# Kernel tuning notes

Measured on AMD Instinct MI355X. Metric: run time of the kernel, lower is better.

## Reference

```python
import jax, jax.numpy as jnp
import numpy as np

K = 3  # kernel_size
P = K // 2


def setup_inputs() -> dict:
    key = jax.random.key(0)
    k1, k2 = jax.random.split(key)
    x = jax.random.normal(k1, (8, 64, 256, 256), dtype=jnp.float32)
    alpha = jnp.full((1, 64, 1, 1), 0.1, dtype=jnp.float32)
    return {"x": x, "alpha": alpha}


def reference(x, alpha):
    # Equivalent to F.unfold(x, K, padding=P) -> abs-diff from center -> sum over K*K -> residual.
    b, c, h, w = x.shape
    xp = jnp.pad(x, ((0, 0), (0, 0), (P, P), (P, P)))  # zero padding, same as F.unfold
    diff_sum = jnp.zeros_like(x)
    for di in range(K):
        for dj in range(K):
            neighbor = xp[:, :, di:di + h, dj:dj + w]
            diff_sum = diff_sum + jnp.abs(x - neighbor)
    return x + alpha * diff_sum
```

## Files before the change

### kernel.cpp

```cpp
#include <hip/hip_runtime.h>


constexpr int H = 256;
constexpr int W = 256;
constexpr int C = 64;

__global__ __launch_bounds__(256, 4) void adc_kernel(
    const float* __restrict__ x,
    const float* __restrict__ alpha,
    float* __restrict__ out)
{
    const int lane = threadIdx.x & 63;
    const int wave = threadIdx.x >> 6;
    const int slab = blockIdx.x;
    const int img  = slab >> 4;
    const int s16  = slab & 15;
    const int y0   = s16 * 16 + wave * 4;
    const int c    = img & (C - 1);

    const float  a    = alpha[c];
    const float* imgp = x   + (long)img * (H * W);
    float*       outp = out + (long)img * (H * W);
    const int    w0   = lane * 4;
    const float* base = imgp + (long)y0 * W + w0;

    const float4 z4 = make_float4(0.f, 0.f, 0.f, 0.f);
    float4 c0 = (y0 > 0)     ? *(const float4*)(base - W)     : z4;
    float4 c1 =                *(const float4*)(base);
    float4 c2 =                *(const float4*)(base + W);
    float4 c3 =                *(const float4*)(base + 2 * W);
    float4 c4 =                *(const float4*)(base + 3 * W);
    float4 c5 = (y0 + 4 < H) ? *(const float4*)(base + 4 * W) : z4;

    __builtin_amdgcn_sched_barrier(0);

    float e[6][6];
#define EXPAND_ROW(k, f)                                            \
    {                                                               \
        e[k][1] = (f).x; e[k][2] = (f).y;                           \
        e[k][3] = (f).z; e[k][4] = (f).w;                           \
        const float lft = __shfl_up((f).w, 1);                      \
        const float rgt = __shfl_down((f).x, 1);                    \
        e[k][0] = (lane == 0)  ? 0.f : lft;     \
        e[k][5] = (lane == 63) ? 0.f : rgt;     \
    }
    EXPAND_ROW(0, c0)
    EXPAND_ROW(1, c1)
    EXPAND_ROW(2, c2)
    EXPAND_ROW(3, c3)
    EXPAND_ROW(4, c4)
    EXPAND_ROW(5, c5)
#undef EXPAND_ROW

#pragma unroll
    for (int o = 0; o < 4; ++o) {
        float4 res;
        float* rp = &res.x;
#pragma unroll
        for (int j = 0; j < 4; ++j) {
            const float xc = e[o + 1][j + 1];
            float s = 0.f;
#pragma unroll
            for (int r = 0; r < 3; ++r)
#pragma unroll
                for (int d = 0; d < 3; ++d)
                    s += fabsf(xc - e[o + r][j + d]);
            rp[j] = fmaf(a, s, xc);
        }
        *(float4*)(outp + (long)(y0 + o) * W + w0) = res;
    }
}

extern "C" void kernel_launch(void* const* d_in, const int* in_sizes, int n_in,
                              void* d_out, int out_size, void* d_ws, size_t ws_size,
                              hipStream_t stream)
{
    const float* x     = (const float*)d_in[0];
    const float* alpha = (const float*)d_in[1];
    float*       out   = (float*)d_out;

    const int grid = 8 * C * (H / 16);
    adc_kernel<<<grid, 256, 0, stream>>>(x, alpha, out);
}
```

Before: 225.5 us.

## Make each wave stream 32 rows with register-rotated halo and prefetch

Each wave now handles 32 rows instead of 4 and walks down them in 8 steps. It keeps a rolling window of six rows in registers and prefetches the next four rows before computing the current ones. This cuts the redundant halo-row loads from 2 per 4 rows to about 2 per 32 rows and overlaps loads with compute. The grid shrinks to 1024 blocks, which lowers parallelism and adds register pressure.

```diff
diff --git a/kernel.cpp b/kernel.cpp
--- a/kernel.cpp
+++ b/kernel.cpp
@@ -12,62 +12,80 @@
 {
     const int lane = threadIdx.x & 63;
     const int wave = threadIdx.x >> 6;
-    const int slab = blockIdx.x;
-    const int img  = slab >> 4;
-    const int s16  = slab & 15;
-    const int y0   = s16 * 16 + wave * 4;
+    const int blk  = blockIdx.x;
+    const int img  = blk >> 1;
+    const int half = blk & 1;
+    const int y0   = half * 128 + wave * 32;
     const int c    = img & (C - 1);
 
-    const float  a    = alpha[c];
-    const float* imgp = x   + (long)img * (H * W);
-    float*       outp = out + (long)img * (H * W);
-    const int    w0   = lane * 4;
-    const float* base = imgp + (long)y0 * W + w0;
+    const float  a     = alpha[c];
+    const float* imgp  = x   + (long)img * (H * W);
+    float*       outp  = out + (long)img * (H * W);
+    const int    w0    = lane * 4;
+    const float* base  = imgp + (long)y0 * W + w0;
+    float*       obase = outp + (long)y0 * W + w0;
 
     const float4 z4 = make_float4(0.f, 0.f, 0.f, 0.f);
-    float4 c0 = (y0 > 0)     ? *(const float4*)(base - W)     : z4;
-    float4 c1 =                *(const float4*)(base);
-    float4 c2 =                *(const float4*)(base + W);
-    float4 c3 =                *(const float4*)(base + 2 * W);
-    float4 c4 =                *(const float4*)(base + 3 * W);
-    float4 c5 = (y0 + 4 < H) ? *(const float4*)(base + 4 * W) : z4;
 
+    float4 c0, c1, c2, c3, c4, c5, n0, n1, n2, n3;
+
+    c0 = (y0 > 0) ? *(const float4*)(base - W) : z4;
+    c1 = *(const float4*)(base);
+    c2 = *(const float4*)(base + W);
+    c3 = *(const float4*)(base + 2 * W);
+    c4 = *(const float4*)(base + 3 * W);
+    c5 = *(const float4*)(base + 4 * W);
     __builtin_amdgcn_sched_barrier(0);
 
-    float e[6][6];
+#pragma unroll
+    for (int t = 0; t < 8; ++t) {
+        if (t < 7) {
+            const int r0 = 4 * t + 5;
+            n0 = *(const float4*)(base + r0 * W);
+            n1 = *(const float4*)(base + (r0 + 1) * W);
+            n2 = *(const float4*)(base + (r0 + 2) * W);
+            n3 = (y0 + r0 + 3 < H)
+                     ? *(const float4*)(base + (r0 + 3) * W) : z4;
+            __builtin_amdgcn_sched_barrier(0);
+        }
+
+        float e[6][6];
 #define EXPAND_ROW(k, f)                                            \
-    {                                                               \
-        e[k][1] = (f).x; e[k][2] = (f).y;                           \
-        e[k][3] = (f).z; e[k][4] = (f).w;                           \
-        const float lft = __shfl_up((f).w, 1);                      \
-        const float rgt = __shfl_down((f).x, 1);                    \
-        e[k][0] = (lane == 0)  ? 0.f : lft;     \
-        e[k][5] = (lane == 63) ? 0.f : rgt;     \
-    }
-    EXPAND_ROW(0, c0)
-    EXPAND_ROW(1, c1)
-    EXPAND_ROW(2, c2)
-    EXPAND_ROW(3, c3)
-    EXPAND_ROW(4, c4)
-    EXPAND_ROW(5, c5)
+        {                                                           \
+            e[k][1] = (f).x; e[k][2] = (f).y;                       \
+            e[k][3] = (f).z; e[k][4] = (f).w;                       \
+            const float lft = __shfl_up((f).w, 1);                  \
+            const float rgt = __shfl_down((f).x, 1);                \
+            e[k][0] = (lane == 0)  ? 0.f : lft;       \
+            e[k][5] = (lane == 63) ? 0.f : rgt;       \
+        }
+        EXPAND_ROW(0, c0)
+        EXPAND_ROW(1, c1)
+        EXPAND_ROW(2, c2)
+        EXPAND_ROW(3, c3)
+        EXPAND_ROW(4, c4)
+        EXPAND_ROW(5, c5)
 #undef EXPAND_ROW
 
 #pragma unroll
-    for (int o = 0; o < 4; ++o) {
-        float4 res;
-        float* rp = &res.x;
+        for (int o = 0; o < 4; ++o) {
+            float4 res;
+            float* rp = &res.x;
 #pragma unroll
-        for (int j = 0; j < 4; ++j) {
-            const float xc = e[o + 1][j + 1];
-            float s = 0.f;
+            for (int j = 0; j < 4; ++j) {
+                const float xc = e[o + 1][j + 1];
+                float s = 0.f;
 #pragma unroll
-            for (int r = 0; r < 3; ++r)
+                for (int r = 0; r < 3; ++r)
 #pragma unroll
-                for (int d = 0; d < 3; ++d)
-                    s += fabsf(xc - e[o + r][j + d]);
-            rp[j] = fmaf(a, s, xc);
+                    for (int d = 0; d < 3; ++d)
+                        s += fabsf(xc - e[o + r][j + d]);
+                rp[j] = fmaf(a, s, xc);
+            }
+            *(float4*)(obase + (4 * t + o) * W) = res;
         }
-        *(float4*)(outp + (long)(y0 + o) * W + w0) = res;
+
+        c0 = c4; c1 = c5; c2 = n0; c3 = n1; c4 = n2; c5 = n3;
     }
 }
 
@@ -79,6 +97,6 @@
     const float* alpha = (const float*)d_in[1];
     float*       out   = (float*)d_out;
 
-    const int grid = 8 * C * (H / 16);
+    const int grid = 8 * C * 2;
     adc_kernel<<<grid, 256, 0, stream>>>(x, alpha, out);
 }
```

Measured after the change: 236.6 us. 1.05x slower.
